# Performance work log

Hardware: AMD Instinct MI355X
Metric: run time of the kernel (lower is better)

Reference implementation:

```python
import jax, jax.numpy as jnp
import numpy as np

B, T, C = 2, 2048, 1024
H, D = 16, 64
SCALE = D ** -0.5


def setup_inputs() -> dict:
    key = jax.random.key(0)
    k1, k2, k3 = jax.random.split(key, 3)
    hidden_states = jax.random.normal(k1, (B, T, C), dtype=jnp.float32)
    # rotary tables: standard RoPE angles, shape (T, D//2)
    inv_freq = 1.0 / (10000.0 ** (np.arange(0, D, 2, dtype=np.float32) / D))
    ang = np.arange(T, dtype=np.float32)[:, None] * inv_freq[None, :]
    cos = jnp.asarray(np.cos(ang))
    sin = jnp.asarray(np.sin(ang))
    qkv_w = jax.random.normal(k2, (3 * H * D, C), dtype=jnp.float32) * 0.02
    qkv_b = jnp.zeros((3 * H * D,), dtype=jnp.float32)
    proj_w = jax.random.normal(k3, (C, H * D), dtype=jnp.float32) * 0.02
    proj_b = jnp.zeros((C,), dtype=jnp.float32)
    return dict(hidden_states=hidden_states, cos=cos, sin=sin,
                qkv_w=qkv_w, qkv_b=qkv_b, proj_w=proj_w, proj_b=proj_b)


def _rotary(x, cos, sin):
    # x: (B, H, T, D); cos/sin: (T, D//2) broadcast over batch and heads
    c = cos[None, None, :, :]
    s = sin[None, None, :, :]
    x1, x2 = x[..., ::2], x[..., 1::2]
    return jnp.concatenate([x1 * c - x2 * s, x1 * s + x2 * c], axis=-1)


def reference(hidden_states, cos, sin, qkv_w, qkv_b, proj_w, proj_b):
    b, t, c = hidden_states.shape
    qkv = hidden_states @ qkv_w.T + qkv_b          # (B, T, 3*H*D)
    q, k, v = jnp.split(qkv, 3, axis=-1)
    # (B, T, H, D) -> (B, H, T, D)
    q = q.reshape(b, t, H, D).transpose(0, 2, 1, 3)
    k = k.reshape(b, t, H, D).transpose(0, 2, 1, 3)
    v = v.reshape(b, t, H, D).transpose(0, 2, 1, 3)
    q = _rotary(q, cos, sin)
    k = _rotary(k, cos, sin)
    scores = jnp.einsum('bhqd,bhkd->bhqk', q, k) * SCALE
    # causal mask: -inf above the diagonal
    mask = jnp.triu(jnp.full((t, t), -jnp.inf, dtype=scores.dtype), k=1)
    scores = scores + mask[None, None, :, :]
    attn = jax.nn.softmax(scores, axis=-1)
    out = jnp.einsum('bhqk,bhkd->bhqd', attn, v)   # (B, H, T, D)
    out = out.transpose(0, 2, 1, 3).reshape(b, t, c)
    return out @ proj_w.T + proj_b
```

## Files before the change

### kernel.cpp

```cpp
#include <hip/hip_runtime.h>
#include <stdint.h>

#define B_ 2
#define T_ 2048
#define C_ 1024
#define H_ 16
#define D_ 64
#define SCALE_L2E 0.1803368801111244f

typedef unsigned short ushort_t;
typedef __attribute__((ext_vector_type(8))) __bf16 bf16x8;
typedef __attribute__((ext_vector_type(4))) float f32x4;
typedef __attribute__((ext_vector_type(4))) unsigned short ushort4_t;

__device__ __forceinline__ float bf2f(ushort_t u) {
    union { unsigned int u; float f; } v; v.u = ((unsigned int)u) << 16; return v.f;
}
__device__ __forceinline__ ushort_t f2bf(float f) {
    union { __bf16 h; ushort_t u; } v; v.h = (__bf16)f; return v.u;
}
__device__ __forceinline__ float fexp2(float x) { return __builtin_amdgcn_exp2f(x); }

__device__ __forceinline__ void gl16(const void* g, void* l) {
    __builtin_amdgcn_global_load_lds(
        (const __attribute__((address_space(1))) void*)g,
        (__attribute__((address_space(3))) void*)l, 16, 0, 0);
}

__device__ __forceinline__ f32x4 mfma16(bf16x8 a, bf16x8 b, f32x4 c) {
    return __builtin_amdgcn_mfma_f32_16x16x32_bf16(a, b, c, 0, 0, 0);
}

__global__ __launch_bounds__(256) void cvt3_kernel(const float* __restrict__ a, ushort_t* __restrict__ oa, int na,
                                                   const float* __restrict__ b, ushort_t* __restrict__ ob, int nb,
                                                   const float* __restrict__ c, ushort_t* __restrict__ oc, int nc) {
    int total4 = (na + nb + nc) >> 2;
    int stride = gridDim.x * blockDim.x;
    for (int i = blockIdx.x * blockDim.x + threadIdx.x; i < total4; i += stride) {
        int e = i << 2;
        const float* src; ushort_t* dst; int off;
        if (e < na) { src = a; dst = oa; off = e; }
        else if (e < na + nb) { src = b; dst = ob; off = e - na; }
        else { src = c; dst = oc; off = e - na - nb; }
        float4 v = *(const float4*)(src + off);
        ushort4_t o;
        o.x = f2bf(v.x); o.y = f2bf(v.y); o.z = f2bf(v.z); o.w = f2bf(v.w);
        *(ushort4_t*)(dst + off) = o;
    }
}

__global__ __launch_bounds__(256) void gemm_proj(const ushort_t* __restrict__ A,
                                                 const ushort_t* __restrict__ Bw,
                                                 const float* __restrict__ bias,
                                                 float* __restrict__ outf,
                                                 int M, int N, int K, int nxt) {
    int q = gridDim.x >> 3;
    int nid = (blockIdx.x & 7) * q + (blockIdx.x >> 3);
    int bx = nid % nxt, by = nid / nxt;

    __shared__ ushort_t sm[18432];
    int tid = threadIdx.x, w = tid >> 6, lane = tid & 63;
    int lr = lane >> 4, lc = lane & 15;
    int wr = w >> 1, wc = w & 1;
    int row0 = by * 64, col0 = bx * 128;

    f32x4 acc[2][4];
#pragma unroll
    for (int mf = 0; mf < 2; ++mf)
#pragma unroll
        for (int nf = 0; nf < 4; ++nf) acc[mf][nf] = (f32x4){0.f, 0.f, 0.f, 0.f};

    auto stageg = [&](int buf, int k0) {
        int base = buf * 6144;
        int rA = tid >> 2, cA = (tid & 3) * 8;
        gl16(A + (size_t)(row0 + rA) * K + k0 + cA, &sm[base + tid * 8]);
#pragma unroll
        for (int j = 0; j < 2; ++j) {
            int idx = j * 256 + tid;
            int rB = idx >> 2, cB = (idx & 3) * 8;
            gl16(Bw + (size_t)(col0 + rB) * K + k0 + cB, &sm[base + 2048 + idx * 8]);
        }
    };

    stageg(0, 0);
    stageg(1, 32);
    asm volatile("s_waitcnt vmcnt(3)" ::: "memory");
    __builtin_amdgcn_s_barrier();

    for (int k0 = 0; k0 < K; k0 += 32) {
        int ks = k0 >> 5;
        int cur = ks % 3;
        bool st = (k0 + 64 < K);
        if (st) stageg((ks + 2) % 3, k0 + 64);
        const ushort_t* As = &sm[cur * 6144];
        const ushort_t* Bs = &sm[cur * 6144 + 2048];
        bf16x8 af[2], bfr[4];
#pragma unroll
        for (int mf = 0; mf < 2; ++mf)
            af[mf] = *(const bf16x8*)&As[(wr * 32 + mf * 16 + lc) * 32 + 8 * lr];
#pragma unroll
        for (int nf = 0; nf < 4; ++nf)
            bfr[nf] = *(const bf16x8*)&Bs[(wc * 64 + nf * 16 + lc) * 32 + 8 * lr];
        __builtin_amdgcn_s_setprio(1);
#pragma unroll
        for (int mf = 0; mf < 2; ++mf)
#pragma unroll
            for (int nf = 0; nf < 4; ++nf)
                acc[mf][nf] = mfma16(af[mf], bfr[nf], acc[mf][nf]);
        __builtin_amdgcn_s_setprio(0);
        if (st) {
            asm volatile("s_waitcnt vmcnt(3)" ::: "memory");
        } else {
            asm volatile("s_waitcnt vmcnt(0)" ::: "memory");
        }
        __builtin_amdgcn_s_barrier();
    }
#pragma unroll
    for (int mf = 0; mf < 2; ++mf)
#pragma unroll
        for (int nf = 0; nf < 4; ++nf) {
            int col = col0 + wc * 64 + nf * 16 + lc;
            float bv = bias[col];
#pragma unroll
            for (int r = 0; r < 4; ++r) {
                int row = row0 + wr * 32 + mf * 16 + 4 * lr + r;
                outf[(size_t)row * N + col] = acc[mf][nf][r] + bv;
            }
        }
}

__global__ __launch_bounds__(256) void gemm_qkv_rope(const ushort_t* __restrict__ A,
                                                     const ushort_t* __restrict__ Bw,
                                                     const float* __restrict__ bias,
                                                     const float* __restrict__ cosT,
                                                     const float* __restrict__ sinT,
                                                     ushort_t* __restrict__ Qr,
                                                     ushort_t* __restrict__ Kr,
                                                     ushort_t* __restrict__ Vt) {
    const int K = 1024;
    int x = blockIdx.x & 7;
    int local = blockIdx.x >> 3;
    int band = x >> 1;
    int half = x & 1;
    int by = band * 8 + (local & 7);
    int bx = half * 12 + (local >> 3);

    __shared__ ushort_t sm[24576];
    int tid = threadIdx.x, w = tid >> 6, lane = tid & 63;
    int lr = lane >> 4, lc = lane & 15;
    int wr = w >> 1, wc = w & 1;
    int row0 = by * 128, col0 = bx * 128;

    f32x4 acc[4][4];
#pragma unroll
    for (int mf = 0; mf < 4; ++mf)
#pragma unroll
        for (int nf = 0; nf < 4; ++nf) acc[mf][nf] = (f32x4){0.f, 0.f, 0.f, 0.f};

    auto stageg = [&](int buf, int k0) {
#pragma unroll
        for (int j = 0; j < 2; ++j) {
            int idx = j * 256 + tid;
            int r = idx >> 2, c = (idx & 3) * 8;
            gl16(A + (size_t)(row0 + r) * K + k0 + c, &sm[buf * 8192 + idx * 8]);
            gl16(Bw + (size_t)(col0 + r) * K + k0 + c, &sm[buf * 8192 + 4096 + idx * 8]);
        }
    };

    stageg(0, 0);
    stageg(1, 32);
    asm volatile("s_waitcnt vmcnt(4)" ::: "memory");
    __builtin_amdgcn_s_barrier();

    for (int k0 = 0; k0 < K; k0 += 32) {
        int ks = k0 >> 5;
        int cur = ks % 3;
        bool st = (k0 + 64 < K);
        if (st) stageg((ks + 2) % 3, k0 + 64);
        const ushort_t* As = &sm[cur * 8192];
        const ushort_t* Bs = &sm[cur * 8192 + 4096];
        bf16x8 af[4], bfr[4];
#pragma unroll
        for (int mf = 0; mf < 4; ++mf)
            af[mf] = *(const bf16x8*)&As[(wr * 64 + mf * 16 + lc) * 32 + 8 * lr];
#pragma unroll
        for (int nf = 0; nf < 4; ++nf)
            bfr[nf] = *(const bf16x8*)&Bs[(wc * 64 + nf * 16 + lc) * 32 + 8 * lr];
        __builtin_amdgcn_s_setprio(1);
#pragma unroll
        for (int mf = 0; mf < 4; ++mf)
#pragma unroll
            for (int nf = 0; nf < 4; ++nf)
                acc[mf][nf] = mfma16(af[mf], bfr[nf], acc[mf][nf]);
        __builtin_amdgcn_s_setprio(0);
        if (st) {
            asm volatile("s_waitcnt vmcnt(4)" ::: "memory");
        } else {
            asm volatile("s_waitcnt vmcnt(0)" ::: "memory");
        }
        __builtin_amdgcn_s_barrier();
    }

    if (bx < 16) {
        const int typ = bx >> 3;
        ushort_t* dstb = typ ? Kr : Qr;
#pragma unroll
        for (int nf = 0; nf < 4; ++nf) {
            int fullc = col0 + wc * 64 + nf * 16 + lc;
            int gc = fullc & 1023;
            int h = gc >> 6;
            int d2 = (gc & 63) >> 1;
            int odd = gc & 1;
            float bv = bias[fullc];
#pragma unroll
            for (int mf = 0; mf < 4; ++mf)
#pragma unroll
                for (int r = 0; r < 4; ++r) {
                    int row = row0 + wr * 64 + mf * 16 + 4 * lr + r;
                    int bb = row >> 11, t = row & 2047;
                    float v = acc[mf][nf][r] + bv;
                    float pv = __shfl_xor(v, 1, 64);
                    float cth = cosT[t * 32 + d2], sth = sinT[t * 32 + d2];
                    float o = odd ? (pv * sth + v * cth) : (v * cth - pv * sth);
                    if (typ == 0) o *= SCALE_L2E;
                    int od = odd ? (d2 + 32) : d2;
                    dstb[((size_t)(bb * H_ + h) * T_ + t) * D_ + od] = f2bf(o);
                }
        }
    } else {
        int bb = row0 >> 11;
        int tb = row0 & 2047;
#pragma unroll 1
        for (int half2 = 0; half2 < 2; ++half2) {
            __syncthreads();
            if (wc == half2) {
#pragma unroll
                for (int nf = 0; nf < 4; ++nf) {
                    int fullc = col0 + wc * 64 + nf * 16 + lc;
                    float bv = bias[fullc];
                    int c = nf * 16 + lc;
#pragma unroll
                    for (int mf = 0; mf < 4; ++mf)
#pragma unroll
                        for (int r = 0; r < 4; ++r) {
                            int tl = wr * 64 + mf * 16 + 4 * lr + r;
                            sm[c * 136 + tl] = f2bf(acc[mf][nf][r] + bv);
                        }
                }
            }
            __syncthreads();
            int h = ((bx - 16) << 1) + half2;
#pragma unroll
            for (int it = 0; it < 8; ++it) {
                int idx = it * 256 + tid;
                int c = idx >> 5, j = idx & 31;
                ushort4_t vv = *(const ushort4_t*)&sm[c * 136 + 4 * j];
                *(ushort4_t*)&Vt[((size_t)(bb * H_ + h) * D_ + c) * T_ + tb + 4 * j] = vv;
            }
        }
    }
}

__global__ __launch_bounds__(256) void attn_kernel(const ushort_t* __restrict__ Qr,
                                                   const ushort_t* __restrict__ Kr,
                                                   const ushort_t* __restrict__ Vt,
                                                   ushort_t* __restrict__ attnb) {
    int id = blockIdx.x;
    int x = id & 7;
    int c = (id >> 3) & 31;
    int g = id >> 8;
    int bh = x + 8 * g;
    int qt;
    if (g == 0) qt = c;
    else if (g == 1) qt = 31 - c;
    else if (g == 2) qt = (c + 16) & 31;
    else qt = 31 - ((c + 16) & 31);
    int b = bh >> 4, h = bh & 15;

    const ushort_t* Qp = Qr + (size_t)bh * T_ * D_;
    const ushort_t* Kp = Kr + (size_t)bh * T_ * D_;
    const ushort_t* Vp = Vt + (size_t)bh * D_ * T_;
    int tid = threadIdx.x, w = tid >> 6, lane = tid & 63;
    int lr = lane >> 4, lc = lane & 15;

    __shared__ ushort_t Ks[2][64 * 64];
    __shared__ ushort_t Vs[2][64 * 64];
    __shared__ ushort_t Ps[4][16 * 64];

    bf16x8 ones;
#pragma unroll
    for (int i = 0; i < 8; ++i) ones[i] = (__bf16)1.0f;

    int srow0 = tid >> 3, sch0 = (tid & 7) ^ (srow0 & 7);
    int srow1 = (256 + tid) >> 3, sch1 = (tid & 7) ^ (srow1 & 7);
    const ushort_t* kg0 = Kp + (size_t)srow0 * D_ + sch0 * 8;
    const ushort_t* kg1 = Kp + (size_t)srow1 * D_ + sch1 * 8;
    const ushort_t* vg0 = Vp + (size_t)srow0 * T_ + sch0 * 8;
    const ushort_t* vg1 = Vp + (size_t)srow1 * T_ + sch1 * 8;
    ushort_t* kl0 = &Ks[0][tid * 8];
    ushort_t* kl1 = &Ks[0][(256 + tid) * 8];
    ushort_t* vl0 = &Vs[0][tid * 8];
    ushort_t* vl1 = &Vs[0][(256 + tid) * 8];

    auto stage = [&](int buf, int kt) {
        size_t koff = (size_t)kt * 64 * D_;
        size_t voff = (size_t)kt * 64;
        size_t lb = (size_t)buf * 4096;
        gl16(kg0 + koff, kl0 + lb);
        gl16(vg0 + voff, vl0 + lb);
        gl16(kg1 + koff, kl1 + lb);
        gl16(vg1 + voff, vl1 + lb);
    };

    int qrow = qt * 64 + w * 16 + lc;
    bf16x8 qf0 = *(const bf16x8*)(Qp + (size_t)qrow * D_ + 8 * lr);
    bf16x8 qf1 = *(const bf16x8*)(Qp + (size_t)qrow * D_ + 32 + 8 * lr);

    float m_s = 0.f;
    f32x4 acc[4], acc_l;
#pragma unroll
    for (int f = 0; f < 4; ++f) acc[f] = (f32x4){0.f, 0.f, 0.f, 0.f};
    acc_l = (f32x4){0.f, 0.f, 0.f, 0.f};

    stage(0, 0);
    asm volatile("s_waitcnt vmcnt(0)" ::: "memory");
    __builtin_amdgcn_s_barrier();

    for (int kt = 0; kt <= qt; ++kt) {
        int cur = kt & 1;
        if (kt < qt) stage(cur ^ 1, kt + 1);
        int t0 = kt * 64;

        f32x4 sv[4];
        __builtin_amdgcn_s_setprio(1);
#pragma unroll
        for (int f = 0; f < 4; ++f) {
            sv[f] = (f32x4){-m_s, -m_s, -m_s, -m_s};
            int row = 16 * f + lc;
#pragma unroll
            for (int kk = 0; kk < 2; ++kk) {
                bf16x8 kf = *(const bf16x8*)&Ks[cur][row * 64 + (((lr + 4 * kk) ^ (row & 7)) * 8)];
                sv[f] = mfma16(kf, kk ? qf1 : qf0, sv[f]);
            }
        }
        __builtin_amdgcn_s_setprio(0);

        float lm = -1e30f;
        if (kt == qt) {
#pragma unroll
            for (int f = 0; f < 4; ++f)
#pragma unroll
                for (int r = 0; r < 4; ++r) {
                    int kg = t0 + 16 * f + 4 * lr + r;
                    float v = sv[f][r];
                    v = (kg > qrow) ? -1e30f : v;
                    sv[f][r] = v;
                    lm = fmaxf(lm, v);
                }
        } else {
#pragma unroll
            for (int f = 0; f < 4; ++f)
#pragma unroll
                for (int r = 0; r < 4; ++r)
                    lm = fmaxf(lm, sv[f][r]);
        }

        if (!__all(lm <= 8.0f)) {
            float tm = fmaxf(lm, __shfl_xor(lm, 16, 64));
            tm = fmaxf(tm, __shfl_xor(tm, 32, 64));
            float d = fmaxf(tm, 0.f);
            m_s += d;
            float alpha = fexp2(-d);
            float ar[4];
#pragma unroll
            for (int r = 0; r < 4; ++r) ar[r] = __shfl(alpha, 4 * lr + r, 64);
#pragma unroll
            for (int r = 0; r < 4; ++r) {
                acc_l[r] *= ar[r];
#pragma unroll
                for (int f = 0; f < 4; ++f) acc[f][r] *= ar[r];
            }
#pragma unroll
            for (int f = 0; f < 4; ++f)
#pragma unroll
                for (int r = 0; r < 4; ++r) sv[f][r] -= d;
        }

#pragma unroll
        for (int f = 0; f < 4; ++f) {
            ushort4_t pk;
            pk.x = f2bf(fexp2(sv[f][0]));
            pk.y = f2bf(fexp2(sv[f][1]));
            pk.z = f2bf(fexp2(sv[f][2]));
            pk.w = f2bf(fexp2(sv[f][3]));
            *(ushort4_t*)&Ps[w][lc * 64 + (((4 * f + lr) ^ (lc & 14)) << 2)] = pk;
        }

        __builtin_amdgcn_s_setprio(1);
#pragma unroll
        for (int kk = 0; kk < 2; ++kk) {
            bf16x8 pf = *(const bf16x8*)&Ps[w][lc * 64 + (((8 * kk + 2 * lr) ^ (lc & 14)) << 2)];
            acc_l = mfma16(pf, ones, acc_l);
#pragma unroll
            for (int f = 0; f < 4; ++f) {
                int vrow = 16 * f + lc;
                bf16x8 vfr = *(const bf16x8*)&Vs[cur][vrow * 64 + (((lr + 4 * kk) ^ (vrow & 7)) * 8)];
                acc[f] = mfma16(pf, vfr, acc[f]);
            }
        }
        __builtin_amdgcn_s_setprio(0);

        asm volatile("s_waitcnt vmcnt(0)" ::: "memory");
        __builtin_amdgcn_s_barrier();
    }

    float inv[4];
#pragma unroll
    for (int r = 0; r < 4; ++r) inv[r] = __builtin_amdgcn_rcpf(acc_l[r]);
#pragma unroll
    for (int f = 0; f < 4; ++f)
#pragma unroll
        for (int r = 0; r < 4; ++r) {
            int t = qt * 64 + w * 16 + 4 * lr + r;
            attnb[((size_t)(b * T_ + t)) * 1024 + h * 64 + 16 * f + lc] =
                f2bf(acc[f][r] * inv[r]);
        }
}

extern "C" void kernel_launch(void* const* d_in, const int* in_sizes, int n_in,
                              void* d_out, int out_size, void* d_ws, size_t ws_size,
                              hipStream_t stream) {
    const float* hs     = (const float*)d_in[0];
    const float* cosp   = (const float*)d_in[1];
    const float* sinp   = (const float*)d_in[2];
    const float* qkv_w  = (const float*)d_in[3];
    const float* qkv_b  = (const float*)d_in[4];
    const float* proj_w = (const float*)d_in[5];
    const float* proj_b = (const float*)d_in[6];
    float* out = (float*)d_out;

    const int M = B_ * T_;
    ushort_t* Xb     = (ushort_t*)d_ws;
    ushort_t* Wqkvb  = Xb + (size_t)M * C_;
    ushort_t* Wprojb = Wqkvb + (size_t)3072 * C_;
    ushort_t* Qr     = Wprojb + (size_t)C_ * C_;
    ushort_t* Kr     = Qr + (size_t)B_ * H_ * T_ * D_;
    ushort_t* Vt     = Kr + (size_t)B_ * H_ * T_ * D_;
    ushort_t* attnb  = Vt + (size_t)B_ * H_ * T_ * D_;

    cvt3_kernel<<<2048, 256, 0, stream>>>(hs, Xb, M * C_,
                                          qkv_w, Wqkvb, 3072 * C_,
                                          proj_w, Wprojb, C_ * C_);

    gemm_qkv_rope<<<768, 256, 0, stream>>>(Xb, Wqkvb, qkv_b, cosp, sinp, Qr, Kr, Vt);

    attn_kernel<<<1024, 256, 0, stream>>>(Qr, Kr, Vt, attnb);

    gemm_proj<<<512, 256, 0, stream>>>(attnb, Wprojb, proj_b, out, M, C_, C_, 8);
}
```

Before: 110.6 us.

## Use persistent attention blocks with atomic work queue, longest tiles first

The attention kernel becomes persistent: 768 blocks each pull (head, query-tile) work items from a per-XCD-slot atomic counter, ordered longest causal tiles first. The goal is better load balance across CUs for the triangular causal workload than the static 1024-block mapping gave. It adds a memset launch, an atomic plus a barrier per item, and a shared counter read that needs an extra barrier to be safe when item_sh is rewritten.

Result: slower. 119.3 us (+7.8%).

```diff
diff --git a/kernel.cpp b/kernel.cpp
--- a/kernel.cpp
+++ b/kernel.cpp
@@ -264,28 +264,16 @@
 __global__ __launch_bounds__(256) void attn_kernel(const ushort_t* __restrict__ Qr,
                                                    const ushort_t* __restrict__ Kr,
                                                    const ushort_t* __restrict__ Vt,
-                                                   ushort_t* __restrict__ attnb) {
-    int id = blockIdx.x;
-    int x = id & 7;
-    int c = (id >> 3) & 31;
-    int g = id >> 8;
-    int bh = x + 8 * g;
-    int qt;
-    if (g == 0) qt = c;
-    else if (g == 1) qt = 31 - c;
-    else if (g == 2) qt = (c + 16) & 31;
-    else qt = 31 - ((c + 16) & 31);
-    int b = bh >> 4, h = bh & 15;
-
-    const ushort_t* Qp = Qr + (size_t)bh * T_ * D_;
-    const ushort_t* Kp = Kr + (size_t)bh * T_ * D_;
-    const ushort_t* Vp = Vt + (size_t)bh * D_ * T_;
+                                                   ushort_t* __restrict__ attnb,
+                                                   unsigned int* __restrict__ cnt) {
+    int x = blockIdx.x & 7;
     int tid = threadIdx.x, w = tid >> 6, lane = tid & 63;
     int lr = lane >> 4, lc = lane & 15;
 
     __shared__ ushort_t Ks[2][64 * 64];
     __shared__ ushort_t Vs[2][64 * 64];
     __shared__ ushort_t Ps[4][16 * 64];
+    __shared__ int item_sh;
 
     bf16x8 ones;
 #pragma unroll
@@ -293,138 +281,152 @@
 
     int srow0 = tid >> 3, sch0 = (tid & 7) ^ (srow0 & 7);
     int srow1 = (256 + tid) >> 3, sch1 = (tid & 7) ^ (srow1 & 7);
-    const ushort_t* kg0 = Kp + (size_t)srow0 * D_ + sch0 * 8;
-    const ushort_t* kg1 = Kp + (size_t)srow1 * D_ + sch1 * 8;
-    const ushort_t* vg0 = Vp + (size_t)srow0 * T_ + sch0 * 8;
-    const ushort_t* vg1 = Vp + (size_t)srow1 * T_ + sch1 * 8;
     ushort_t* kl0 = &Ks[0][tid * 8];
     ushort_t* kl1 = &Ks[0][(256 + tid) * 8];
     ushort_t* vl0 = &Vs[0][tid * 8];
     ushort_t* vl1 = &Vs[0][(256 + tid) * 8];
 
-    auto stage = [&](int buf, int kt) {
-        size_t koff = (size_t)kt * 64 * D_;
-        size_t voff = (size_t)kt * 64;
-        size_t lb = (size_t)buf * 4096;
-        gl16(kg0 + koff, kl0 + lb);
-        gl16(vg0 + voff, vl0 + lb);
-        gl16(kg1 + koff, kl1 + lb);
-        gl16(vg1 + voff, vl1 + lb);
-    };
-
-    int qrow = qt * 64 + w * 16 + lc;
-    bf16x8 qf0 = *(const bf16x8*)(Qp + (size_t)qrow * D_ + 8 * lr);
-    bf16x8 qf1 = *(const bf16x8*)(Qp + (size_t)qrow * D_ + 32 + 8 * lr);
-
-    float m_s = 0.f;
-    f32x4 acc[4], acc_l;
-#pragma unroll
-    for (int f = 0; f < 4; ++f) acc[f] = (f32x4){0.f, 0.f, 0.f, 0.f};
-    acc_l = (f32x4){0.f, 0.f, 0.f, 0.f};
-
-    stage(0, 0);
-    asm volatile("s_waitcnt vmcnt(0)" ::: "memory");
-    __builtin_amdgcn_s_barrier();
-
-    for (int kt = 0; kt <= qt; ++kt) {
-        int cur = kt & 1;
-        if (kt < qt) stage(cur ^ 1, kt + 1);
-        int t0 = kt * 64;
-
-        f32x4 sv[4];
-        __builtin_amdgcn_s_setprio(1);
-#pragma unroll
-        for (int f = 0; f < 4; ++f) {
-            sv[f] = (f32x4){-m_s, -m_s, -m_s, -m_s};
-            int row = 16 * f + lc;
-#pragma unroll
-            for (int kk = 0; kk < 2; ++kk) {
-                bf16x8 kf = *(const bf16x8*)&Ks[cur][row * 64 + (((lr + 4 * kk) ^ (row & 7)) * 8)];
-                sv[f] = mfma16(kf, kk ? qf1 : qf0, sv[f]);
-            }
-        }
-        __builtin_amdgcn_s_setprio(0);
-
-        float lm = -1e30f;
-        if (kt == qt) {
-#pragma unroll
-            for (int f = 0; f < 4; ++f)
-#pragma unroll
-                for (int r = 0; r < 4; ++r) {
-                    int kg = t0 + 16 * f + 4 * lr + r;
-                    float v = sv[f][r];
-                    v = (kg > qrow) ? -1e30f : v;
-                    sv[f][r] = v;
-                    lm = fmaxf(lm, v);
-                }
-        } else {
-#pragma unroll
-            for (int f = 0; f < 4; ++f)
-#pragma unroll
-                for (int r = 0; r < 4; ++r)
-                    lm = fmaxf(lm, sv[f][r]);
-        }
-
-        if (!__all(lm <= 8.0f)) {
-            float tm = fmaxf(lm, __shfl_xor(lm, 16, 64));
-            tm = fmaxf(tm, __shfl_xor(tm, 32, 64));
-            float d = fmaxf(tm, 0.f);
-            m_s += d;
-            float alpha = fexp2(-d);
-            float ar[4];
-#pragma unroll
-            for (int r = 0; r < 4; ++r) ar[r] = __shfl(alpha, 4 * lr + r, 64);
-#pragma unroll
-            for (int r = 0; r < 4; ++r) {
-                acc_l[r] *= ar[r];
-#pragma unroll
-                for (int f = 0; f < 4; ++f) acc[f][r] *= ar[r];
-            }
-#pragma unroll
-            for (int f = 0; f < 4; ++f)
-#pragma unroll
-                for (int r = 0; r < 4; ++r) sv[f][r] -= d;
-        }
-
-#pragma unroll
-        for (int f = 0; f < 4; ++f) {
-            ushort4_t pk;
-            pk.x = f2bf(fexp2(sv[f][0]));
-            pk.y = f2bf(fexp2(sv[f][1]));
-            pk.z = f2bf(fexp2(sv[f][2]));
-            pk.w = f2bf(fexp2(sv[f][3]));
-            *(ushort4_t*)&Ps[w][lc * 64 + (((4 * f + lr) ^ (lc & 14)) << 2)] = pk;
-        }
-
-        __builtin_amdgcn_s_setprio(1);
-#pragma unroll
-        for (int kk = 0; kk < 2; ++kk) {
-            bf16x8 pf = *(const bf16x8*)&Ps[w][lc * 64 + (((8 * kk + 2 * lr) ^ (lc & 14)) << 2)];
-            acc_l = mfma16(pf, ones, acc_l);
-#pragma unroll
-            for (int f = 0; f < 4; ++f) {
-                int vrow = 16 * f + lc;
-                bf16x8 vfr = *(const bf16x8*)&Vs[cur][vrow * 64 + (((lr + 4 * kk) ^ (vrow & 7)) * 8)];
-                acc[f] = mfma16(pf, vfr, acc[f]);
-            }
-        }
-        __builtin_amdgcn_s_setprio(0);
-
+    for (;;) {
+        if (tid == 0) item_sh = (int)atomicAdd(&cnt[x], 1u);
+        __syncthreads();
+        int t = item_sh;
+        if (t >= 128) break;
+        int qt = 31 - (t >> 2);
+        int bh = x + 8 * (t & 3);
+        int b = bh >> 4, h = bh & 15;
+
+        const ushort_t* Qp = Qr + (size_t)bh * T_ * D_;
+        const ushort_t* Kp = Kr + (size_t)bh * T_ * D_;
+        const ushort_t* Vp = Vt + (size_t)bh * D_ * T_;
+        const ushort_t* kg0 = Kp + (size_t)srow0 * D_ + sch0 * 8;
+        const ushort_t* kg1 = Kp + (size_t)srow1 * D_ + sch1 * 8;
+        const ushort_t* vg0 = Vp + (size_t)srow0 * T_ + sch0 * 8;
+        const ushort_t* vg1 = Vp + (size_t)srow1 * T_ + sch1 * 8;
+
+        auto stage = [&](int buf, int kt) {
+            size_t koff = (size_t)kt * 64 * D_;
+            size_t voff = (size_t)kt * 64;
+            size_t lb = (size_t)buf * 4096;
+            gl16(kg0 + koff, kl0 + lb);
+            gl16(vg0 + voff, vl0 + lb);
+            gl16(kg1 + koff, kl1 + lb);
+            gl16(vg1 + voff, vl1 + lb);
+        };
+
+        int qrow = qt * 64 + w * 16 + lc;
+        bf16x8 qf0 = *(const bf16x8*)(Qp + (size_t)qrow * D_ + 8 * lr);
+        bf16x8 qf1 = *(const bf16x8*)(Qp + (size_t)qrow * D_ + 32 + 8 * lr);
+
+        float m_s = 0.f;
+        f32x4 acc[4], acc_l;
+#pragma unroll
+        for (int f = 0; f < 4; ++f) acc[f] = (f32x4){0.f, 0.f, 0.f, 0.f};
+        acc_l = (f32x4){0.f, 0.f, 0.f, 0.f};
+
+        stage(0, 0);
         asm volatile("s_waitcnt vmcnt(0)" ::: "memory");
         __builtin_amdgcn_s_barrier();
+
+        for (int kt = 0; kt <= qt; ++kt) {
+            int cur = kt & 1;
+            if (kt < qt) stage(cur ^ 1, kt + 1);
+            int t0 = kt * 64;
+
+            f32x4 sv[4];
+            __builtin_amdgcn_s_setprio(1);
+#pragma unroll
+            for (int f = 0; f < 4; ++f) {
+                sv[f] = (f32x4){-m_s, -m_s, -m_s, -m_s};
+                int row = 16 * f + lc;
+#pragma unroll
+                for (int kk = 0; kk < 2; ++kk) {
+                    bf16x8 kf = *(const bf16x8*)&Ks[cur][row * 64 + (((lr + 4 * kk) ^ (row & 7)) * 8)];
+                    sv[f] = mfma16(kf, kk ? qf1 : qf0, sv[f]);
+                }
+            }
+            __builtin_amdgcn_s_setprio(0);
+
+            float lm = -1e30f;
+            if (kt == qt) {
+#pragma unroll
+                for (int f = 0; f < 4; ++f)
+#pragma unroll
+                    for (int r = 0; r < 4; ++r) {
+                        int kg = t0 + 16 * f + 4 * lr + r;
+                        float v = sv[f][r];
+                        v = (kg > qrow) ? -1e30f : v;
+                        sv[f][r] = v;
+                        lm = fmaxf(lm, v);
+                    }
+            } else {
+#pragma unroll
+                for (int f = 0; f < 4; ++f)
+#pragma unroll
+                    for (int r = 0; r < 4; ++r)
+                        lm = fmaxf(lm, sv[f][r]);
+            }
+
+            if (!__all(lm <= 8.0f)) {
+                float tm = fmaxf(lm, __shfl_xor(lm, 16, 64));
+                tm = fmaxf(tm, __shfl_xor(tm, 32, 64));
+                float d = fmaxf(tm, 0.f);
+                m_s += d;
+                float alpha = fexp2(-d);
+                float ar[4];
+#pragma unroll
+                for (int r = 0; r < 4; ++r) ar[r] = __shfl(alpha, 4 * lr + r, 64);
+#pragma unroll
+                for (int r = 0; r < 4; ++r) {
+                    acc_l[r] *= ar[r];
+#pragma unroll
+                    for (int f = 0; f < 4; ++f) acc[f][r] *= ar[r];
+                }
+#pragma unroll
+                for (int f = 0; f < 4; ++f)
+#pragma unroll
+                    for (int r = 0; r < 4; ++r) sv[f][r] -= d;
+            }
+
+#pragma unroll
+            for (int f = 0; f < 4; ++f) {
+                ushort4_t pk;
+                pk.x = f2bf(fexp2(sv[f][0]));
+                pk.y = f2bf(fexp2(sv[f][1]));
+                pk.z = f2bf(fexp2(sv[f][2]));
+                pk.w = f2bf(fexp2(sv[f][3]));
+                *(ushort4_t*)&Ps[w][lc * 64 + (((4 * f + lr) ^ (lc & 14)) << 2)] = pk;
+            }
+
+            __builtin_amdgcn_s_setprio(1);
+#pragma unroll
+            for (int kk = 0; kk < 2; ++kk) {
+                bf16x8 pf = *(const bf16x8*)&Ps[w][lc * 64 + (((8 * kk + 2 * lr) ^ (lc & 14)) << 2)];
+                acc_l = mfma16(pf, ones, acc_l);
+#pragma unroll
+                for (int f = 0; f < 4; ++f) {
+                    int vrow = 16 * f + lc;
+                    bf16x8 vfr = *(const bf16x8*)&Vs[cur][vrow * 64 + (((lr + 4 * kk) ^ (vrow & 7)) * 8)];
+                    acc[f] = mfma16(pf, vfr, acc[f]);
+                }
+            }
+            __builtin_amdgcn_s_setprio(0);
+
+            asm volatile("s_waitcnt vmcnt(0)" ::: "memory");
+            __builtin_amdgcn_s_barrier();
+        }
+
+        float inv[4];
+#pragma unroll
+        for (int r = 0; r < 4; ++r) inv[r] = __builtin_amdgcn_rcpf(acc_l[r]);
+#pragma unroll
+        for (int f = 0; f < 4; ++f)
+#pragma unroll
+            for (int r = 0; r < 4; ++r) {
+                int tq = qt * 64 + w * 16 + 4 * lr + r;
+                attnb[((size_t)(b * T_ + tq)) * 1024 + h * 64 + 16 * f + lc] =
+                    f2bf(acc[f][r] * inv[r]);
+            }
     }
-
-    float inv[4];
-#pragma unroll
-    for (int r = 0; r < 4; ++r) inv[r] = __builtin_amdgcn_rcpf(acc_l[r]);
-#pragma unroll
-    for (int f = 0; f < 4; ++f)
-#pragma unroll
-        for (int r = 0; r < 4; ++r) {
-            int t = qt * 64 + w * 16 + 4 * lr + r;
-            attnb[((size_t)(b * T_ + t)) * 1024 + h * 64 + 16 * f + lc] =
-                f2bf(acc[f][r] * inv[r]);
-        }
 }
 
 extern "C" void kernel_launch(void* const* d_in, const int* in_sizes, int n_in,
@@ -447,6 +449,7 @@
     ushort_t* Kr     = Qr + (size_t)B_ * H_ * T_ * D_;
     ushort_t* Vt     = Kr + (size_t)B_ * H_ * T_ * D_;
     ushort_t* attnb  = Vt + (size_t)B_ * H_ * T_ * D_;
+    unsigned int* cnt = (unsigned int*)(attnb + (size_t)M * C_);
 
     cvt3_kernel<<<2048, 256, 0, stream>>>(hs, Xb, M * C_,
                                           qkv_w, Wqkvb, 3072 * C_,
@@ -454,7 +457,9 @@
 
     gemm_qkv_rope<<<768, 256, 0, stream>>>(Xb, Wqkvb, qkv_b, cosp, sinp, Qr, Kr, Vt);
 
-    attn_kernel<<<1024, 256, 0, stream>>>(Qr, Kr, Vt, attnb);
+    hipMemsetAsync((void*)cnt, 0, 32, stream);
+
+    attn_kernel<<<768, 256, 0, stream>>>(Qr, Kr, Vt, attnb, cnt);
 
     gemm_proj<<<512, 256, 0, stream>>>(attnb, Wprojb, proj_b, out, M, C_, C_, 8);
 }
```
